# Performance work log

Measured on AMD Instinct MI355X. Metric: run time of the kernel, lower is better.

## Reference

```python
import jax, jax.numpy as jnp
import numpy as np

EMBED_DIM = 128
NUM_HEADS = 4
HEAD_DIM = EMBED_DIM // NUM_HEADS


def setup_inputs() -> dict:
    key = jax.random.key(0)
    ks = jax.random.split(key, 12)
    B, N, D = 4, 4096, EMBED_DIM
    s = 1.0 / np.sqrt(D)
    inp = {
        "query": jax.random.normal(ks[0], (B, N, D), dtype=jnp.float32),
        "key": jax.random.normal(ks[1], (B, N, D), dtype=jnp.float32),
        "value": jax.random.normal(ks[2], (B, N, D), dtype=jnp.float32),
        "Wq": jax.random.uniform(ks[3], (D, D), jnp.float32, -s, s),
        "bq": jax.random.uniform(ks[4], (D,), jnp.float32, -s, s),
        "Wk": jax.random.uniform(ks[5], (D, D), jnp.float32, -s, s),
        "bk": jax.random.uniform(ks[6], (D,), jnp.float32, -s, s),
        "Wv": jax.random.uniform(ks[7], (D, D), jnp.float32, -s, s),
        "bv": jax.random.uniform(ks[8], (D,), jnp.float32, -s, s),
        "Wo": jax.random.uniform(ks[9], (D, D), jnp.float32, -s, s),
        "bo": jax.random.uniform(ks[10], (D,), jnp.float32, -s, s),
    }
    return inp


def reference(query, key, value, Wq, bq, Wk, bk, Wv, bv, Wo, bo):
    B, N, D = query.shape
    H, Dh = NUM_HEADS, HEAD_DIM
    scale = Dh ** -0.5
    # Linear projections (torch Linear: x @ W.T + b), split heads -> [B, H, N, Dh]
    Q = (query @ Wq.T + bq).reshape(B, N, H, Dh).transpose(0, 2, 1, 3)
    K = (key @ Wk.T + bk).reshape(B, N, H, Dh).transpose(0, 2, 1, 3)
    V = (value @ Wv.T + bv).reshape(B, N, H, Dh).transpose(0, 2, 1, 3)
    # Attention scores [B, H, N, N]
    scores = jnp.einsum('bhqd,bhkd->bhqk', Q, K) * scale
    attn = jax.nn.softmax(scores, axis=-1)
    ctx = jnp.einsum('bhqk,bhkd->bhqd', attn, V)  # [B, H, N, Dh]
    ctx = ctx.transpose(0, 2, 1, 3).reshape(B, N, D)
    return ctx @ Wo.T + bo
```

## Files before the change

kernel.cpp:

```cpp
#include <hip/hip_runtime.h>
#include <hip/hip_bf16.h>

#define N_SEQ 4096
#define DIM   128
#define NH    4
#define DH    32
#define BATCH 4

#define QSCALE 0.25503495870989204f

typedef __bf16 bf16x8 __attribute__((ext_vector_type(8)));
typedef __bf16 bf16x2 __attribute__((ext_vector_type(2)));
typedef __bf16 bf16x4 __attribute__((ext_vector_type(4)));
typedef float  f32x4  __attribute__((ext_vector_type(4)));

#define MFMA(a, b, c) __builtin_amdgcn_mfma_f32_16x16x32_bf16((a), (b), (c), 0, 0, 0)

static __device__ __forceinline__ bf16x8 cvt8(const float* __restrict__ p) {
    const float4* f4 = reinterpret_cast<const float4*>(p);
    float4 a = f4[0], b = f4[1];
    bf16x8 r;
    r[0] = (__bf16)a.x; r[1] = (__bf16)a.y; r[2] = (__bf16)a.z; r[3] = (__bf16)a.w;
    r[4] = (__bf16)b.x; r[5] = (__bf16)b.y; r[6] = (__bf16)b.z; r[7] = (__bf16)b.w;
    return r;
}

static __device__ __forceinline__ f32x4 exp4(f32x4 s) {
    f32x4 r;
    r[0] = __builtin_amdgcn_exp2f(s[0]);
    r[1] = __builtin_amdgcn_exp2f(s[1]);
    r[2] = __builtin_amdgcn_exp2f(s[2]);
    r[3] = __builtin_amdgcn_exp2f(s[3]);
    return r;
}

static __device__ __forceinline__ bf16x8 pack8(f32x4 a, f32x4 b) {
    bf16x8 o;
    o[0] = (__bf16)a[0]; o[1] = (__bf16)a[1];
    o[2] = (__bf16)a[2]; o[3] = (__bf16)a[3];
    o[4] = (__bf16)b[0]; o[5] = (__bf16)b[1];
    o[6] = (__bf16)b[2]; o[7] = (__bf16)b[3];
    return o;
}

__global__ __launch_bounds__(256) void proj_qkv(
    const float* __restrict__ xq, const float* __restrict__ xk, const float* __restrict__ xv,
    const float* __restrict__ Wq, const float* __restrict__ Wk, const float* __restrict__ Wv,
    const float* __restrict__ bq, const float* __restrict__ bk, const float* __restrict__ bv,
    __bf16* __restrict__ Qs, __bf16* __restrict__ Kb, __bf16* __restrict__ Vt)
{
    __shared__ __align__(16) char wlds[34816];
    const int z = blockIdx.z;
    const float* x    = (z == 0) ? xq : ((z == 1) ? xk : xv);
    const float* Wf   = (z == 0) ? Wq : ((z == 1) ? Wk : Wv);
    const float* bias = (z == 0) ? bq : ((z == 1) ? bk : bv);
    const int b    = blockIdx.y;
    const int tid  = threadIdx.x;
    const int wave = tid >> 6, lane = tid & 63;
    const int quad = lane >> 4, l15 = lane & 15;
    const int n0   = blockIdx.x * 64 + wave * 16;

    {
        const int r = tid >> 1, half = tid & 1;
        const float* wsrc = Wf + r * DIM + half * 64;
        char* wdst = wlds + r * 272 + half * 128;
        #pragma unroll
        for (int i = 0; i < 8; i++)
            *(bf16x8*)(wdst + i * 16) = cvt8(wsrc + i * 8);
    }

    bf16x8 a[4];
    const float* xrow = x + (b * N_SEQ + n0 + l15) * DIM + quad * 8;
    a[0] = cvt8(xrow);      a[1] = cvt8(xrow + 32);
    a[2] = cvt8(xrow + 64); a[3] = cvt8(xrow + 96);
    __syncthreads();

    const int n = n0 + l15;
    for (int t = 0; t < 8; t++) {
        const char* wr = wlds + (t * 16 + l15) * 272 + quad * 16;
        bf16x8 w0 = *(const bf16x8*)(wr);
        bf16x8 w1 = *(const bf16x8*)(wr + 64);
        bf16x8 w2 = *(const bf16x8*)(wr + 128);
        bf16x8 w3 = *(const bf16x8*)(wr + 192);

        f32x4 acc = {0.f, 0.f, 0.f, 0.f};
        acc = MFMA(w0, a[0], acc);
        acc = MFMA(w1, a[1], acc);
        acc = MFMA(w2, a[2], acc);
        acc = MFMA(w3, a[3], acc);

        const int d0 = t * 16 + quad * 4;
        if (z == 0) {
            const int h = d0 >> 5, dh0 = d0 & 31;
            bf16x4 q4;
            #pragma unroll
            for (int r = 0; r < 4; r++)
                q4[r] = (__bf16)((acc[r] + bias[d0 + r]) * QSCALE);
            *(bf16x4*)(Qs + ((b * NH + h) * N_SEQ + n) * DH + dh0) = q4;
        } else if (z == 1) {
            const int h = d0 >> 5, dh0 = d0 & 31;
            bf16x4 k4;
            #pragma unroll
            for (int r = 0; r < 4; r++)
                k4[r] = (__bf16)(acc[r] + bias[d0 + r]);
            *(bf16x4*)(Kb + ((b * NH + h) * N_SEQ + n) * DH + dh0) = k4;
        } else {
            const int nl = n & 63;
            const int np = (n & ~63) | (nl & 35) | ((nl & 12) << 1) | ((nl & 16) >> 2);
            #pragma unroll
            for (int r = 0; r < 4; r++) {
                const int d = d0 + r, h = d >> 5, dh = d & 31;
                Vt[((b * NH + h) * DH + dh) * N_SEQ + np] = (__bf16)(acc[r] + bias[d]);
            }
        }
    }
}

__global__ __launch_bounds__(256, 2) void flash_attn(
    const __bf16* __restrict__ Qs, const __bf16* __restrict__ Kb,
    const __bf16* __restrict__ Vt, __bf16* __restrict__ ctxb)
{
    __shared__ __align__(16) char smem[77824];
    char* const Kbase = smem;
    char* const Vbase = smem + 40960;

    const int bid  = blockIdx.x;
    const int bh   = bid & 15;
    const int qc   = bid >> 4;
    const int tid  = threadIdx.x;
    const int wave = tid >> 6, lane = tid & 63;
    const int quad = lane >> 4, l15 = lane & 15;
    const int qh   = wave & 1, kh = wave >> 1;
    const int n0   = qc * 128 + qh * 64;
    const int KH   = 2048;

    const __bf16* Qp = Qs + (bh * N_SEQ + n0) * DH;
    bf16x8 qf[4];
    #pragma unroll
    for (int q = 0; q < 4; q++)
        qf[q] = *(const bf16x8*)(Qp + (q * 16 + l15) * DH + quad * 8);

    bf16x8 ones;
    #pragma unroll
    for (int i = 0; i < 8; i++) ones[i] = (__bf16)1.0f;

    const int r_ = tid >> 2, c_ = tid & 3;
    const __bf16* gK = Kb + (size_t)bh * N_SEQ * DH + r_ * DH + c_ * 8;
    const __bf16* gV = Vt + ((size_t)bh * DH + (tid >> 3)) * N_SEQ + (tid & 7) * 8;
    const int kofsK = r_ * 80 + c_ * 16;
    const int kofsV = (tid >> 3) * 144 + (tid & 7) * 16;

    {
        #pragma unroll
        for (int g = 0; g < 2; g++) {
            #pragma unroll
            for (int t = 0; t < 2; t++) {
                bf16x8 kr = *(const bf16x8*)(gK + (size_t)(g * KH + t * 64) * DH);
                bf16x8 vr = *(const bf16x8*)(gV + g * KH + t * 64);
                *(bf16x8*)(Kbase + g * 20480 + t * 5120 + kofsK) = kr;
                *(bf16x8*)(Vbase + g * 18432 + t * 4608 + kofsV) = vr;
            }
        }
    }
    __syncthreads();

    char* const Kme = Kbase + kh * 20480;
    char* const Vme = Vbase + kh * 18432;

    f32x4 c[4][2];
    f32x4 cl[4];
    const f32x4 z4 = {0.f,0.f,0.f,0.f};
    #pragma unroll
    for (int q = 0; q < 4; q++) { c[q][0] = z4; c[q][1] = z4; cl[q] = z4; }

    for (int kbb = 0; kbb < KH / 128; kbb++) {
        const int cur = kbb & 1;
        const char* Kc = Kme + cur * 10240;
        const char* Vc = Vme + cur * 9216;

        const int kn = (kbb + 1) & (KH / 128 - 1);
        bf16x8 krn[2][2], vrn[2][2];
        #pragma unroll
        for (int g = 0; g < 2; g++) {
            #pragma unroll
            for (int t = 0; t < 2; t++) {
                krn[g][t] = *(const bf16x8*)(gK + (size_t)(g * KH + kn * 128 + t * 64) * DH);
                vrn[g][t] = *(const bf16x8*)(gV + g * KH + kn * 128 + t * 64);
            }
        }

        bf16x8 kfa[2][4], vfa[2][4];
        #pragma unroll
        for (int t = 0; t < 2; t++) {
            const char* Kt  = Kc + t * 5120;
            const char* Vtl = Vc + t * 4608;
            #pragma unroll
            for (int i = 0; i < 4; i++)
                kfa[t][i] = *(const bf16x8*)(Kt + (i * 16 + l15) * 80 + quad * 16);
            vfa[t][0] = *(const bf16x8*)(Vtl + l15 * 144 + quad * 16);
            vfa[t][1] = *(const bf16x8*)(Vtl + (16 + l15) * 144 + quad * 16);
            vfa[t][2] = *(const bf16x8*)(Vtl + l15 * 144 + 64 + quad * 16);
            vfa[t][3] = *(const bf16x8*)(Vtl + (16 + l15) * 144 + 64 + quad * 16);
        }

        #pragma unroll
        for (int t = 0; t < 2; t++) {
            bf16x8 pf[4][2];
            #pragma unroll
            for (int q = 0; q < 4; q++) {
                __builtin_amdgcn_s_setprio(1);
                f32x4 sa = MFMA(kfa[t][0], qf[q], z4);
                f32x4 sb = MFMA(kfa[t][1], qf[q], z4);
                f32x4 sc = MFMA(kfa[t][2], qf[q], z4);
                f32x4 sd = MFMA(kfa[t][3], qf[q], z4);
                __builtin_amdgcn_s_setprio(0);
                f32x4 ea = exp4(sa), eb = exp4(sb), ec = exp4(sc), ed = exp4(sd);
                pf[q][0] = pack8(ea, eb);
                pf[q][1] = pack8(ec, ed);
            }

            __builtin_amdgcn_s_setprio(1);
            #pragma unroll
            for (int q = 0; q < 4; q++) {
                c[q][0] = MFMA(vfa[t][0], pf[q][0], c[q][0]);
                c[q][1] = MFMA(vfa[t][1], pf[q][0], c[q][1]);
                c[q][0] = MFMA(vfa[t][2], pf[q][1], c[q][0]);
                c[q][1] = MFMA(vfa[t][3], pf[q][1], c[q][1]);
                cl[q]   = MFMA(ones, pf[q][0], cl[q]);
                cl[q]   = MFMA(ones, pf[q][1], cl[q]);
            }
            __builtin_amdgcn_s_setprio(0);
        }

        #pragma unroll
        for (int g = 0; g < 2; g++) {
            #pragma unroll
            for (int t = 0; t < 2; t++) {
                *(bf16x8*)(Kbase + g * 20480 + (cur ^ 1) * 10240 + t * 5120 + kofsK) = krn[g][t];
                *(bf16x8*)(Vbase + g * 18432 + (cur ^ 1) * 9216 + t * 4608 + kofsV) = vrn[g][t];
            }
        }
        __syncthreads();
    }

    if (kh == 1) {
        char* dst = smem + (qh * 64 + lane) * 144;
        #pragma unroll
        for (int q = 0; q < 4; q++) {
            *(f32x4*)(dst + (q * 2 + 0) * 16) = c[q][0];
            *(f32x4*)(dst + (q * 2 + 1) * 16) = c[q][1];
        }
        f32x4 lv = {cl[0][0], cl[1][0], cl[2][0], cl[3][0]};
        *(f32x4*)(dst + 128) = lv;
    }
    __syncthreads();
    if (kh == 0) {
        const char* src = smem + (qh * 64 + lane) * 144;
        f32x4 lp = *(const f32x4*)(src + 128);
        const int b = bh >> 2, h = bh & 3;
        #pragma unroll
        for (int q = 0; q < 4; q++) {
            c[q][0] += *(const f32x4*)(src + (q * 2 + 0) * 16);
            c[q][1] += *(const f32x4*)(src + (q * 2 + 1) * 16);
            const float inv = 1.0f / (cl[q][0] + lp[q]);
            const int qg = n0 + q * 16 + l15;
            __bf16* dst = ctxb + ((size_t)(b * N_SEQ + qg)) * DIM + h * DH + quad * 4;
            #pragma unroll
            for (int dt = 0; dt < 2; dt++) {
                f32x4 cc = c[q][dt];
                bf16x2 e0 = {(__bf16)(cc[0] * inv), (__bf16)(cc[1] * inv)};
                bf16x2 e1 = {(__bf16)(cc[2] * inv), (__bf16)(cc[3] * inv)};
                *(bf16x2*)(dst + dt * 16)     = e0;
                *(bf16x2*)(dst + dt * 16 + 2) = e1;
            }
        }
    }
}

__global__ __launch_bounds__(256) void out_proj(
    const __bf16* __restrict__ ctxb, const float* __restrict__ Wo,
    const float* __restrict__ bo, float* __restrict__ out)
{
    __shared__ __align__(16) char wlds[34816];
    const int b    = blockIdx.y;
    const int tid  = threadIdx.x;
    const int wave = tid >> 6, lane = tid & 63;
    const int quad = lane >> 4, l15 = lane & 15;
    const int n0   = blockIdx.x * 64 + wave * 16;

    {
        const int r = tid >> 1, half = tid & 1;
        const float* wsrc = Wo + r * DIM + half * 64;
        char* wdst = wlds + r * 272 + half * 128;
        #pragma unroll
        for (int i = 0; i < 8; i++)
            *(bf16x8*)(wdst + i * 16) = cvt8(wsrc + i * 8);
    }

    bf16x8 a[4];
    const __bf16* crow = ctxb + (b * N_SEQ + n0 + l15) * DIM + quad * 8;
    a[0] = *(const bf16x8*)(crow);
    a[1] = *(const bf16x8*)(crow + 32);
    a[2] = *(const bf16x8*)(crow + 64);
    a[3] = *(const bf16x8*)(crow + 96);
    __syncthreads();

    const int n = n0 + l15;
    for (int t = 0; t < 8; t++) {
        const char* wr = wlds + (t * 16 + l15) * 272 + quad * 16;
        bf16x8 w0 = *(const bf16x8*)(wr);
        bf16x8 w1 = *(const bf16x8*)(wr + 64);
        bf16x8 w2 = *(const bf16x8*)(wr + 128);
        bf16x8 w3 = *(const bf16x8*)(wr + 192);

        f32x4 acc = {0.f, 0.f, 0.f, 0.f};
        acc = MFMA(w0, a[0], acc);
        acc = MFMA(w1, a[1], acc);
        acc = MFMA(w2, a[2], acc);
        acc = MFMA(w3, a[3], acc);

        const int d0 = t * 16 + quad * 4;
        float4 o;
        o.x = acc[0] + bo[d0];
        o.y = acc[1] + bo[d0 + 1];
        o.z = acc[2] + bo[d0 + 2];
        o.w = acc[3] + bo[d0 + 3];
        *(float4*)(out + (b * N_SEQ + n) * DIM + d0) = o;
    }
}

extern "C" void kernel_launch(void* const* d_in, const int* in_sizes, int n_in,
                              void* d_out, int out_size, void* d_ws, size_t ws_size,
                              hipStream_t stream)
{
    const float* query = (const float*)d_in[0];
    const float* key   = (const float*)d_in[1];
    const float* value = (const float*)d_in[2];
    const float* Wq = (const float*)d_in[3];
    const float* bq = (const float*)d_in[4];
    const float* Wk = (const float*)d_in[5];
    const float* bk = (const float*)d_in[6];
    const float* Wv = (const float*)d_in[7];
    const float* bv = (const float*)d_in[8];
    const float* Wo = (const float*)d_in[9];
    const float* bo = (const float*)d_in[10];
    float* out = (float*)d_out;

    char* ws = (char*)d_ws;
    const size_t e = (size_t)BATCH * N_SEQ * DIM;
    __bf16* Qs   = (__bf16*)(ws);
    __bf16* Kb   = (__bf16*)(ws + 2 * e);
    __bf16* Vt   = (__bf16*)(ws + 4 * e);
    __bf16* ctxb = (__bf16*)(ws + 6 * e);

    proj_qkv<<<dim3(64, BATCH, 3), 256, 0, stream>>>(
        query, key, value, Wq, Wk, Wv, bq, bk, bv, Qs, Kb, Vt);
    flash_attn<<<dim3(512), 256, 0, stream>>>(Qs, Kb, Vt, ctxb);
    out_proj<<<dim3(64, BATCH), 256, 0, stream>>>(ctxb, Wo, bo, out);
}
```

Baseline: 146.7 us.

## Software-pipeline QK and PV MFMAs across sub-tiles to overlap exp with matrix ops

Restructures the inner attention loop so the PV accumulation for the previous 64-key sub-tile is interleaved with the QK^T MFMAs of the current sub-tile, carrying P fragments and V fragments across iterations with an epilogue drain. The aim is to hide the exp/pack VALU latency behind MFMA work instead of serialising score, exp and accumulate phases. In exchange it raises register pressure from the extra live pfA/pfB and vfB_prev fragments, which may lower occupancy or cause spills.

```diff
diff --git a/kernel.cpp b/kernel.cpp
--- a/kernel.cpp
+++ b/kernel.cpp
@@ -173,6 +173,18 @@
     #pragma unroll
     for (int q = 0; q < 4; q++) { c[q][0] = z4; c[q][1] = z4; cl[q] = z4; }
 
+    bf16x8 pfA[4][2], pfB[4][2];
+    bf16x8 vfB_prev[4];
+    {
+        bf16x8 zb;
+        #pragma unroll
+        for (int i = 0; i < 8; i++) zb[i] = (__bf16)0.0f;
+        #pragma unroll
+        for (int q = 0; q < 4; q++) { pfA[q][0]=zb; pfA[q][1]=zb; pfB[q][0]=zb; pfB[q][1]=zb; }
+        #pragma unroll
+        for (int i = 0; i < 4; i++) vfB_prev[i] = zb;
+    }
+
     for (int kbb = 0; kbb < KH / 128; kbb++) {
         const int cur = kbb & 1;
         const char* Kc = Kme + cur * 10240;
@@ -204,33 +216,47 @@
         }
 
         #pragma unroll
-        for (int t = 0; t < 2; t++) {
-            bf16x8 pf[4][2];
-            #pragma unroll
-            for (int q = 0; q < 4; q++) {
-                __builtin_amdgcn_s_setprio(1);
-                f32x4 sa = MFMA(kfa[t][0], qf[q], z4);
-                f32x4 sb = MFMA(kfa[t][1], qf[q], z4);
-                f32x4 sc = MFMA(kfa[t][2], qf[q], z4);
-                f32x4 sd = MFMA(kfa[t][3], qf[q], z4);
-                __builtin_amdgcn_s_setprio(0);
-                f32x4 ea = exp4(sa), eb = exp4(sb), ec = exp4(sc), ed = exp4(sd);
-                pf[q][0] = pack8(ea, eb);
-                pf[q][1] = pack8(ec, ed);
-            }
-
+        for (int q = 0; q < 4; q++) {
             __builtin_amdgcn_s_setprio(1);
-            #pragma unroll
-            for (int q = 0; q < 4; q++) {
-                c[q][0] = MFMA(vfa[t][0], pf[q][0], c[q][0]);
-                c[q][1] = MFMA(vfa[t][1], pf[q][0], c[q][1]);
-                c[q][0] = MFMA(vfa[t][2], pf[q][1], c[q][0]);
-                c[q][1] = MFMA(vfa[t][3], pf[q][1], c[q][1]);
-                cl[q]   = MFMA(ones, pf[q][0], cl[q]);
-                cl[q]   = MFMA(ones, pf[q][1], cl[q]);
+            f32x4 sa = MFMA(kfa[0][0], qf[q], z4);
+            f32x4 sb = MFMA(kfa[0][1], qf[q], z4);
+            f32x4 sc = MFMA(kfa[0][2], qf[q], z4);
+            f32x4 sd = MFMA(kfa[0][3], qf[q], z4);
+            if (kbb > 0) {
+                c[q][0] = MFMA(vfB_prev[0], pfB[q][0], c[q][0]);
+                c[q][1] = MFMA(vfB_prev[1], pfB[q][0], c[q][1]);
+                c[q][0] = MFMA(vfB_prev[2], pfB[q][1], c[q][0]);
+                c[q][1] = MFMA(vfB_prev[3], pfB[q][1], c[q][1]);
+                cl[q]   = MFMA(ones, pfB[q][0], cl[q]);
+                cl[q]   = MFMA(ones, pfB[q][1], cl[q]);
             }
             __builtin_amdgcn_s_setprio(0);
-        }
+            f32x4 ea = exp4(sa), eb = exp4(sb), ec = exp4(sc), ed = exp4(sd);
+            pfA[q][0] = pack8(ea, eb);
+            pfA[q][1] = pack8(ec, ed);
+        }
+
+        #pragma unroll
+        for (int q = 0; q < 4; q++) {
+            __builtin_amdgcn_s_setprio(1);
+            f32x4 sa = MFMA(kfa[1][0], qf[q], z4);
+            f32x4 sb = MFMA(kfa[1][1], qf[q], z4);
+            f32x4 sc = MFMA(kfa[1][2], qf[q], z4);
+            f32x4 sd = MFMA(kfa[1][3], qf[q], z4);
+            c[q][0] = MFMA(vfa[0][0], pfA[q][0], c[q][0]);
+            c[q][1] = MFMA(vfa[0][1], pfA[q][0], c[q][1]);
+            c[q][0] = MFMA(vfa[0][2], pfA[q][1], c[q][0]);
+            c[q][1] = MFMA(vfa[0][3], pfA[q][1], c[q][1]);
+            cl[q]   = MFMA(ones, pfA[q][0], cl[q]);
+            cl[q]   = MFMA(ones, pfA[q][1], cl[q]);
+            __builtin_amdgcn_s_setprio(0);
+            f32x4 ea = exp4(sa), eb = exp4(sb), ec = exp4(sc), ed = exp4(sd);
+            pfB[q][0] = pack8(ea, eb);
+            pfB[q][1] = pack8(ec, ed);
+        }
+
+        #pragma unroll
+        for (int i = 0; i < 4; i++) vfB_prev[i] = vfa[1][i];
 
         #pragma unroll
         for (int g = 0; g < 2; g++) {
@@ -241,6 +267,16 @@
             }
         }
         __syncthreads();
+    }
+
+    #pragma unroll
+    for (int q = 0; q < 4; q++) {
+        c[q][0] = MFMA(vfB_prev[0], pfB[q][0], c[q][0]);
+        c[q][1] = MFMA(vfB_prev[1], pfB[q][0], c[q][1]);
+        c[q][0] = MFMA(vfB_prev[2], pfB[q][1], c[q][0]);
+        c[q][1] = MFMA(vfB_prev[3], pfB[q][1], c[q][1]);
+        cl[q]   = MFMA(ones, pfB[q][0], cl[q]);
+        cl[q]   = MFMA(ones, pfB[q][1], cl[q]);
     }
 
     if (kh == 1) {
```

Result: no change. 147.7 us (+0.7%).
